# Optimization experiments

Measured on AMD Instinct MI355X. Metric: run time of the kernel, lower is better.

The kernel has to match this reference:

```python
import jax, jax.numpy as jnp
import numpy as np

B, S, F = 128, 1024, 512
H = 32          # LSTM hidden size
G = 4 * H       # i, f, g, o gates


def setup_inputs() -> dict:
    key = jax.random.key(0)
    ks = jax.random.split(key, 12)
    sc = lambda fan_in: 1.0 / np.sqrt(fan_in)
    return {
        "x":  jax.random.normal(ks[0], (B, S, F), dtype=jnp.float32),
        "W1": jax.random.normal(ks[1], (F, 32), dtype=jnp.float32) * sc(F),
        "b1": jnp.zeros((32,), jnp.float32),
        "W2": jax.random.normal(ks[2], (32, 64), dtype=jnp.float32) * sc(32),
        "b2": jnp.zeros((64,), jnp.float32),
        "Wx": jax.random.normal(ks[3], (64, G), dtype=jnp.float32) * sc(64),
        "Wh": jax.random.normal(ks[4], (H, G), dtype=jnp.float32) * sc(H),
        "bl": jnp.zeros((G,), jnp.float32),
        "W3": jax.random.normal(ks[5], (H, 64), dtype=jnp.float32) * sc(H),
        "b3": jnp.zeros((64,), jnp.float32),
        "W4": jax.random.normal(ks[6], (64, 512), dtype=jnp.float32) * sc(64),
        "b4": jnp.zeros((512,), jnp.float32),
    }


def _lstm_scan(xg, Wh):
    # xg: [B, S, 4H] precomputed input-side gate pre-activations (incl. bias)
    def step(carry, xt):
        c, h = carry
        g = xt + h @ Wh                      # [B, 4H]
        i, f, gg, o = jnp.split(g, 4, axis=-1)
        i, f, o = jax.nn.sigmoid(i), jax.nn.sigmoid(f), jax.nn.sigmoid(o)
        c = f * c + i * jnp.tanh(gg)
        h = o * jnp.tanh(c)
        return (c, h), h

    c0 = jnp.zeros((xg.shape[0], H), xg.dtype)
    h0 = jnp.zeros((xg.shape[0], H), xg.dtype)
    _, hs = jax.lax.scan(step, (c0, h0), jnp.swapaxes(xg, 0, 1))  # hs: [S, B, H]
    return jnp.swapaxes(hs, 0, 1)            # [B, S, H]


def reference(x, W1, b1, W2, b2, Wx, Wh, bl, W3, b3, W4, b4):
    h = jnp.tanh(x @ W1 + b1)                # [B, S, 32]
    h = jnp.tanh(h @ W2 + b2)                # [B, S, 64]
    xg = h @ Wx + bl                          # [B, S, 4H] input-side gates
    hs = _lstm_scan(xg, Wh)                   # [B, S, H]
    h = jnp.tanh(hs @ W3 + b3)                # [B, S, 64]
    return h @ W4 + b4                        # [B, S, 512]
```

## Files before the change

### kernel.cpp

```cpp
#include <hip/hip_runtime.h>
#include <hip/hip_bf16.h>


typedef __attribute__((ext_vector_type(8))) __bf16 bf16x8;
typedef __attribute__((ext_vector_type(4))) __bf16 bf16x4;
typedef __attribute__((ext_vector_type(4))) float floatx4;
typedef __attribute__((ext_vector_type(2))) float floatx2;

__global__ __launch_bounds__(256) void k_mlp_xg(
    const float* __restrict__ x,  const float* __restrict__ W1, const float* __restrict__ b1,
    const float* __restrict__ W2, const float* __restrict__ b2,
    const float* __restrict__ Wx, const float* __restrict__ bl,
    float* __restrict__ xg)
{
    __shared__ __align__(16) char smem[51712];
    __bf16* w1T = (__bf16*)smem;
    __bf16* w2T = (__bf16*)smem;
    __bf16* wxT = (__bf16*)(smem + 5120);
    __bf16* xsh = (__bf16*)(smem + 33280);
    __bf16* xsl = (__bf16*)(smem + 42496);
    __bf16* h1s = (__bf16*)(smem + 33280);
    __bf16* h2s = (__bf16*)(smem + 38400);

    const int tid  = threadIdx.x;
    const int lane = tid & 63, w = tid >> 6;
    const int quad = lane >> 4, col = lane & 15;
    const int row0 = blockIdx.x * 64;
    const int m     = w * 16 + col;
    const int rbase = w * 16 + quad * 4;
    const floatx4 fzero = {0.f, 0.f, 0.f, 0.f};

    for (int i = tid; i < 512 * 32; i += 256) {
        int k = i >> 5, n = i & 31;
        w1T[n * 520 + k] = (__bf16)W1[i];
    }
    auto stage_x = [&](int kc) {
        for (int i4 = tid; i4 < 1024; i4 += 256) {
            int f = i4 << 2; int r = f >> 6, cc = f & 63;
            float4 v = *(const float4*)(x + (size_t)(row0 + r) * 512 + kc * 64 + cc);
            __bf16 h0 = (__bf16)v.x, h1 = (__bf16)v.y, h2 = (__bf16)v.z, h3 = (__bf16)v.w;
            bf16x4 hi = {h0, h1, h2, h3};
            bf16x4 lo = {(__bf16)(v.x - (float)h0), (__bf16)(v.y - (float)h1),
                         (__bf16)(v.z - (float)h2), (__bf16)(v.w - (float)h3)};
            *(bf16x4*)(xsh + r * 72 + cc) = hi;
            *(bf16x4*)(xsl + r * 72 + cc) = lo;
        }
    };
    stage_x(0);
    __syncthreads();

    floatx4 acc1[2] = {fzero, fzero};
    for (int kc = 0; kc < 8; ++kc) {
#pragma unroll
        for (int ks = 0; ks < 2; ++ks) {
            int ko = ks * 32 + quad * 8;
            bf16x8 ah = *(const bf16x8*)(xsh + m * 72 + ko);
            bf16x8 al = *(const bf16x8*)(xsl + m * 72 + ko);
            int kg = kc * 64 + ko;
#pragma unroll
            for (int nt = 0; nt < 2; ++nt) {
                bf16x8 bfr = *(const bf16x8*)(w1T + (nt * 16 + col) * 520 + kg);
                acc1[nt] = __builtin_amdgcn_mfma_f32_16x16x32_bf16(ah, bfr, acc1[nt], 0, 0, 0);
                acc1[nt] = __builtin_amdgcn_mfma_f32_16x16x32_bf16(al, bfr, acc1[nt], 0, 0, 0);
            }
        }
        if (kc < 7) { __syncthreads(); stage_x(kc + 1); __syncthreads(); }
    }
    __syncthreads();

#pragma unroll
    for (int nt = 0; nt < 2; ++nt) {
        float bb = b1[nt * 16 + col];
#pragma unroll
        for (int r = 0; r < 4; ++r)
            h1s[(rbase + r) * 40 + nt * 16 + col] = (__bf16)tanhf(acc1[nt][r] + bb);
    }
    for (int i = tid; i < 32 * 64; i += 256)  { int k = i >> 6, n = i & 63;  w2T[n * 40 + k] = (__bf16)W2[i]; }
    for (int i = tid; i < 64 * 128; i += 256) { int k = i >> 7, n = i & 127; wxT[n * 72 + k] = (__bf16)Wx[i]; }
    __syncthreads();

    bf16x8 a2 = *(const bf16x8*)(h1s + m * 40 + quad * 8);
    floatx4 acc2[4];
#pragma unroll
    for (int nt = 0; nt < 4; ++nt) {
        bf16x8 bfr = *(const bf16x8*)(w2T + (nt * 16 + col) * 40 + quad * 8);
        acc2[nt] = __builtin_amdgcn_mfma_f32_16x16x32_bf16(a2, bfr, fzero, 0, 0, 0);
    }
#pragma unroll
    for (int nt = 0; nt < 4; ++nt) {
        float bb = b2[nt * 16 + col];
#pragma unroll
        for (int r = 0; r < 4; ++r)
            h2s[(rbase + r) * 72 + nt * 16 + col] = (__bf16)tanhf(acc2[nt][r] + bb);
    }

    floatx4 acc3[8];
#pragma unroll
    for (int nt = 0; nt < 8; ++nt) acc3[nt] = fzero;
#pragma unroll
    for (int ks = 0; ks < 2; ++ks) {
        int ko = ks * 32 + quad * 8;
        bf16x8 a3 = *(const bf16x8*)(h2s + m * 72 + ko);
#pragma unroll
        for (int nt = 0; nt < 8; ++nt) {
            bf16x8 bfr = *(const bf16x8*)(wxT + (nt * 16 + col) * 72 + ko);
            acc3[nt] = __builtin_amdgcn_mfma_f32_16x16x32_bf16(a3, bfr, acc3[nt], 0, 0, 0);
        }
    }
#pragma unroll
    for (int nt = 0; nt < 8; ++nt) {
        float bb = bl[nt * 16 + col];
#pragma unroll
        for (int r = 0; r < 4; ++r)
            xg[(size_t)(row0 + rbase + r) * 128 + nt * 16 + col] = acc3[nt][r] + bb;
    }
}

#define RLANE(v, k) __uint_as_float(__builtin_amdgcn_readlane(__float_as_uint(v), (k)))

__global__ __launch_bounds__(64) void k_lstm(
    const float* __restrict__ xg, const float* __restrict__ Wh,
    float* __restrict__ hs)
{
    __shared__ __align__(16) float xbuf[3][32 * 128];

    const int b = blockIdx.x;
    const int l = threadIdx.x;
    const float* xgb = xg + (size_t)b * 1024 * 128;
    float* hsb = hs + (size_t)b * 1024 * 32;

    floatx2 wh[32];
#pragma unroll
    for (int k = 0; k < 32; ++k)
        wh[k] = floatx2{Wh[k * 128 + l], Wh[k * 128 + 64 + l]};

    const float sc1 = (l < 32) ? 2.0f : 1.0f;
    const float m1  = (l < 32) ? 2.0f : 1.0f;
    const float c1  = (l < 32) ? -1.0f : 0.0f;

    auto stage_chunk = [&](int cidx) {
        const float* src = xgb + (size_t)cidx * 4096 + l * 4;
        float* dst = &xbuf[cidx % 3][0];
#pragma unroll
        for (int i = 0; i < 16; ++i)
            __builtin_amdgcn_global_load_lds(src + i * 256, dst + i * 256, 16, 0, 0);
    };

    stage_chunk(0); stage_chunk(1); stage_chunk(2);
    asm volatile("s_waitcnt vmcnt(16)" ::: "memory");

    float c = 0.f, h = 0.f;

    float xr0[4], xr1[4];
#pragma unroll
    for (int p = 0; p < 4; ++p) {
        xr0[p] = xbuf[0][p * 128 + l];
        xr1[p] = xbuf[0][p * 128 + 64 + l];
    }

#pragma unroll 1
    for (int ch = 0; ch < 32; ++ch) {
        const float* bufc = xbuf[ch % 3];
        const float* bufn = xbuf[(ch + 1) % 3];
#pragma unroll 1
        for (int s = 0; s < 32; s += 4) {
#pragma unroll
            for (int u = 0; u < 4; ++u) {
                const int tc = ch * 32 + s + u;
                float x0 = xr0[u], x1 = xr1[u];
                {
                    int rn = s + u + 4;
                    const float* p = (rn < 32) ? (bufc + rn * 128) : (bufn + (rn - 32) * 128);
                    xr0[u] = p[l];
                    xr1[u] = p[64 + l];
                }
                floatx2 pa = {x0, x1};
                floatx2 pb = {0.f, 0.f}, pc = {0.f, 0.f}, pd = {0.f, 0.f};
#pragma unroll
                for (int k = 0; k < 32; k += 4) {
                    float h0 = RLANE(h, k);
                    float h1 = RLANE(h, k + 1);
                    float h2 = RLANE(h, k + 2);
                    float h3 = RLANE(h, k + 3);
                    pa += wh[k]     * h0;
                    pb += wh[k + 1] * h1;
                    pc += wh[k + 2] * h2;
                    pd += wh[k + 3] * h3;
                }
                floatx2 pe = (pa + pb) + (pc + pd);
                float pre0 = pe.x;
                float pre1 = pe.y;
                float a0 = __builtin_amdgcn_rcpf(1.0f + __expf(-pre0));
                float s1 = __builtin_amdgcn_rcpf(1.0f + __expf(-sc1 * pre1));
                float a1 = __builtin_fmaf(s1, m1, c1);
                float f_ = __shfl(a0, l ^ 32);
                float o_ = __shfl(a1, l ^ 32);
                c = f_ * c + a0 * a1;
                float e = __expf(-2.0f * c);
                float th = (1.0f - e) * __builtin_amdgcn_rcpf(1.0f + e);
                h = o_ * th;
                if (l < 32) hsb[tc * 32 + l] = h;
            }
        }
        if (ch + 3 < 32) {
            stage_chunk(ch + 3);
            asm volatile("s_waitcnt vmcnt(16)" ::: "memory");
        } else {
            asm volatile("s_waitcnt vmcnt(0)" ::: "memory");
        }
    }
}

__global__ __launch_bounds__(256) void k_tail(
    const float* __restrict__ hs, const float* __restrict__ W3, const float* __restrict__ b3,
    const float* __restrict__ W4, const float* __restrict__ b4,
    float* __restrict__ out)
{
    __shared__ __align__(16) char smem[37888];
    __bf16* hss = (__bf16*)smem;
    __bf16* w3T = (__bf16*)(smem + 5120);
    __bf16* h3s = (__bf16*)(smem + 10240);
    __bf16* w4T = (__bf16*)(smem + 19456);

    const int tid  = threadIdx.x;
    const int lane = tid & 63, w = tid >> 6;
    const int quad = lane >> 4, col = lane & 15;
    const int row0 = blockIdx.x * 64;
    const int m     = w * 16 + col;
    const int rbase = w * 16 + quad * 4;
    const floatx4 fzero = {0.f, 0.f, 0.f, 0.f};

    for (int i4 = tid; i4 < 512; i4 += 256) {
        int f = i4 << 2; int r = f >> 5, cc = f & 31;
        float4 v = *(const float4*)(hs + (size_t)(row0 + r) * 32 + cc);
        bf16x4 hv = {(__bf16)v.x, (__bf16)v.y, (__bf16)v.z, (__bf16)v.w};
        *(bf16x4*)(hss + r * 40 + cc) = hv;
    }
    for (int i = tid; i < 32 * 64; i += 256) { int k = i >> 6, n = i & 63; w3T[n * 40 + k] = (__bf16)W3[i]; }
    __syncthreads();

    bf16x8 a3 = *(const bf16x8*)(hss + m * 40 + quad * 8);
    floatx4 acc3[4];
#pragma unroll
    for (int nt = 0; nt < 4; ++nt) {
        bf16x8 bfr = *(const bf16x8*)(w3T + (nt * 16 + col) * 40 + quad * 8);
        acc3[nt] = __builtin_amdgcn_mfma_f32_16x16x32_bf16(a3, bfr, fzero, 0, 0, 0);
    }
#pragma unroll
    for (int nt = 0; nt < 4; ++nt) {
        float bb = b3[nt * 16 + col];
#pragma unroll
        for (int r = 0; r < 4; ++r)
            h3s[(rbase + r) * 72 + nt * 16 + col] = (__bf16)tanhf(acc3[nt][r] + bb);
    }

    for (int oc = 0; oc < 4; ++oc) {
        __syncthreads();
        for (int i4 = tid; i4 < 2048; i4 += 256) {
            int f = i4 << 2; int k = f >> 7, cc = f & 127;
            float4 v = *(const float4*)(W4 + (size_t)k * 512 + oc * 128 + cc);
            w4T[(cc + 0) * 72 + k] = (__bf16)v.x;
            w4T[(cc + 1) * 72 + k] = (__bf16)v.y;
            w4T[(cc + 2) * 72 + k] = (__bf16)v.z;
            w4T[(cc + 3) * 72 + k] = (__bf16)v.w;
        }
        __syncthreads();

        floatx4 acc4[8];
#pragma unroll
        for (int nt = 0; nt < 8; ++nt) acc4[nt] = fzero;
#pragma unroll
        for (int ks = 0; ks < 2; ++ks) {
            int ko = ks * 32 + quad * 8;
            bf16x8 a4 = *(const bf16x8*)(h3s + m * 72 + ko);
#pragma unroll
            for (int nt = 0; nt < 8; ++nt) {
                bf16x8 bfr = *(const bf16x8*)(w4T + (nt * 16 + col) * 72 + ko);
                acc4[nt] = __builtin_amdgcn_mfma_f32_16x16x32_bf16(a4, bfr, acc4[nt], 0, 0, 0);
            }
        }
#pragma unroll
        for (int nt = 0; nt < 8; ++nt) {
            float bb = b4[oc * 128 + nt * 16 + col];
#pragma unroll
            for (int r = 0; r < 4; ++r)
                out[(size_t)(row0 + rbase + r) * 512 + oc * 128 + nt * 16 + col] = acc4[nt][r] + bb;
        }
    }
}

extern "C" void kernel_launch(void* const* d_in, const int* in_sizes, int n_in,
                              void* d_out, int out_size, void* d_ws, size_t ws_size,
                              hipStream_t stream)
{
    (void)in_sizes; (void)n_in; (void)out_size;
    const float* x  = (const float*)d_in[0];
    const float* W1 = (const float*)d_in[1];
    const float* b1 = (const float*)d_in[2];
    const float* W2 = (const float*)d_in[3];
    const float* b2 = (const float*)d_in[4];
    const float* Wx = (const float*)d_in[5];
    const float* Wh = (const float*)d_in[6];
    const float* bl = (const float*)d_in[7];
    const float* W3 = (const float*)d_in[8];
    const float* b3 = (const float*)d_in[9];
    const float* W4 = (const float*)d_in[10];
    const float* b4 = (const float*)d_in[11];
    float* out = (float*)d_out;

    const size_t hsElems = (size_t)128 * 1024 * 32;
    const size_t xgElems = (size_t)128 * 1024 * 128;
    float* hs = (float*)d_ws;
    float* xg = (ws_size >= (hsElems + xgElems) * sizeof(float))
                    ? hs + hsElems
                    : out;

    k_mlp_xg<<<2048, 256, 0, stream>>>(x, W1, b1, W2, b2, Wx, bl, xg);
    k_lstm<<<128, 64, 0, stream>>>(xg, Wh, hs);
    k_tail<<<2048, 256, 0, stream>>>(hs, W3, b3, W4, b4, out);
}
```

Baseline: 830.9 us.

## Load x directly into MFMA fragments and enlarge tail kernel row tiles

Result: no change. 818.9 us (-1.4%).

```diff
diff --git a/kernel.cpp b/kernel.cpp
--- a/kernel.cpp
+++ b/kernel.cpp
@@ -13,12 +13,10 @@
     const float* __restrict__ Wx, const float* __restrict__ bl,
     float* __restrict__ xg)
 {
-    __shared__ __align__(16) char smem[51712];
+    __shared__ __align__(16) char smem[47616];
     __bf16* w1T = (__bf16*)smem;
     __bf16* w2T = (__bf16*)smem;
     __bf16* wxT = (__bf16*)(smem + 5120);
-    __bf16* xsh = (__bf16*)(smem + 33280);
-    __bf16* xsl = (__bf16*)(smem + 42496);
     __bf16* h1s = (__bf16*)(smem + 33280);
     __bf16* h2s = (__bf16*)(smem + 38400);
 
@@ -34,29 +32,23 @@
         int k = i >> 5, n = i & 31;
         w1T[n * 520 + k] = (__bf16)W1[i];
     }
-    auto stage_x = [&](int kc) {
-        for (int i4 = tid; i4 < 1024; i4 += 256) {
-            int f = i4 << 2; int r = f >> 6, cc = f & 63;
-            float4 v = *(const float4*)(x + (size_t)(row0 + r) * 512 + kc * 64 + cc);
-            __bf16 h0 = (__bf16)v.x, h1 = (__bf16)v.y, h2 = (__bf16)v.z, h3 = (__bf16)v.w;
-            bf16x4 hi = {h0, h1, h2, h3};
-            bf16x4 lo = {(__bf16)(v.x - (float)h0), (__bf16)(v.y - (float)h1),
-                         (__bf16)(v.z - (float)h2), (__bf16)(v.w - (float)h3)};
-            *(bf16x4*)(xsh + r * 72 + cc) = hi;
-            *(bf16x4*)(xsl + r * 72 + cc) = lo;
-        }
-    };
-    stage_x(0);
     __syncthreads();
 
+    const float* xrow = x + (size_t)(row0 + m) * 512;
     floatx4 acc1[2] = {fzero, fzero};
     for (int kc = 0; kc < 8; ++kc) {
 #pragma unroll
         for (int ks = 0; ks < 2; ++ks) {
-            int ko = ks * 32 + quad * 8;
-            bf16x8 ah = *(const bf16x8*)(xsh + m * 72 + ko);
-            bf16x8 al = *(const bf16x8*)(xsl + m * 72 + ko);
-            int kg = kc * 64 + ko;
+            int kg = kc * 64 + ks * 32 + quad * 8;
+            float4 v0 = *(const float4*)(xrow + kg);
+            float4 v1 = *(const float4*)(xrow + kg + 4);
+            __bf16 e0 = (__bf16)v0.x, e1 = (__bf16)v0.y, e2 = (__bf16)v0.z, e3 = (__bf16)v0.w;
+            __bf16 e4 = (__bf16)v1.x, e5 = (__bf16)v1.y, e6 = (__bf16)v1.z, e7 = (__bf16)v1.w;
+            bf16x8 ah = {e0, e1, e2, e3, e4, e5, e6, e7};
+            bf16x8 al = {(__bf16)(v0.x - (float)e0), (__bf16)(v0.y - (float)e1),
+                         (__bf16)(v0.z - (float)e2), (__bf16)(v0.w - (float)e3),
+                         (__bf16)(v1.x - (float)e4), (__bf16)(v1.y - (float)e5),
+                         (__bf16)(v1.z - (float)e6), (__bf16)(v1.w - (float)e7)};
 #pragma unroll
             for (int nt = 0; nt < 2; ++nt) {
                 bf16x8 bfr = *(const bf16x8*)(w1T + (nt * 16 + col) * 520 + kg);
@@ -64,7 +56,6 @@
                 acc1[nt] = __builtin_amdgcn_mfma_f32_16x16x32_bf16(al, bfr, acc1[nt], 0, 0, 0);
             }
         }
-        if (kc < 7) { __syncthreads(); stage_x(kc + 1); __syncthreads(); }
     }
     __syncthreads();
 
@@ -211,26 +202,24 @@
     }
 }
 
-__global__ __launch_bounds__(256) void k_tail(
+__global__ __launch_bounds__(256, 2) void k_tail(
     const float* __restrict__ hs, const float* __restrict__ W3, const float* __restrict__ b3,
     const float* __restrict__ W4, const float* __restrict__ b4,
     float* __restrict__ out)
 {
-    __shared__ __align__(16) char smem[37888];
-    __bf16* hss = (__bf16*)smem;
-    __bf16* w3T = (__bf16*)(smem + 5120);
-    __bf16* h3s = (__bf16*)(smem + 10240);
-    __bf16* w4T = (__bf16*)(smem + 19456);
+    __shared__ __align__(16) char smem[62464];
+    __bf16* h3s = (__bf16*)smem;
+    __bf16* hss = (__bf16*)(smem + 36864);
+    __bf16* w4T = (__bf16*)(smem + 36864);
+    __bf16* w3T = (__bf16*)(smem + 57344);
 
     const int tid  = threadIdx.x;
     const int lane = tid & 63, w = tid >> 6;
     const int quad = lane >> 4, col = lane & 15;
-    const int row0 = blockIdx.x * 64;
-    const int m     = w * 16 + col;
-    const int rbase = w * 16 + quad * 4;
+    const int row0 = blockIdx.x * 256;
     const floatx4 fzero = {0.f, 0.f, 0.f, 0.f};
 
-    for (int i4 = tid; i4 < 512; i4 += 256) {
+    for (int i4 = tid; i4 < 2048; i4 += 256) {
         int f = i4 << 2; int r = f >> 5, cc = f & 31;
         float4 v = *(const float4*)(hs + (size_t)(row0 + r) * 32 + cc);
         bf16x4 hv = {(__bf16)v.x, (__bf16)v.y, (__bf16)v.z, (__bf16)v.w};
@@ -239,52 +228,75 @@
     for (int i = tid; i < 32 * 64; i += 256) { int k = i >> 6, n = i & 63; w3T[n * 40 + k] = (__bf16)W3[i]; }
     __syncthreads();
 
-    bf16x8 a3 = *(const bf16x8*)(hss + m * 40 + quad * 8);
-    floatx4 acc3[4];
-#pragma unroll
-    for (int nt = 0; nt < 4; ++nt) {
-        bf16x8 bfr = *(const bf16x8*)(w3T + (nt * 16 + col) * 40 + quad * 8);
-        acc3[nt] = __builtin_amdgcn_mfma_f32_16x16x32_bf16(a3, bfr, fzero, 0, 0, 0);
-    }
-#pragma unroll
-    for (int nt = 0; nt < 4; ++nt) {
-        float bb = b3[nt * 16 + col];
-#pragma unroll
-        for (int r = 0; r < 4; ++r)
-            h3s[(rbase + r) * 72 + nt * 16 + col] = (__bf16)tanhf(acc3[nt][r] + bb);
+#pragma unroll
+    for (int mt = 0; mt < 4; ++mt) {
+        const int m     = w * 64 + mt * 16 + col;
+        const int rbase = w * 64 + mt * 16 + quad * 4;
+        bf16x8 a3 = *(const bf16x8*)(hss + m * 40 + quad * 8);
+        floatx4 acc3[4];
+#pragma unroll
+        for (int nt = 0; nt < 4; ++nt) {
+            bf16x8 bfr = *(const bf16x8*)(w3T + (nt * 16 + col) * 40 + quad * 8);
+            acc3[nt] = __builtin_amdgcn_mfma_f32_16x16x32_bf16(a3, bfr, fzero, 0, 0, 0);
+        }
+#pragma unroll
+        for (int nt = 0; nt < 4; ++nt) {
+            float bb = b3[nt * 16 + col];
+#pragma unroll
+            for (int r = 0; r < 4; ++r)
+                h3s[(rbase + r) * 72 + nt * 16 + col] = (__bf16)tanhf(acc3[nt][r] + bb);
+        }
     }
 
     for (int oc = 0; oc < 4; ++oc) {
         __syncthreads();
-        for (int i4 = tid; i4 < 2048; i4 += 256) {
-            int f = i4 << 2; int k = f >> 7, cc = f & 127;
-            float4 v = *(const float4*)(W4 + (size_t)k * 512 + oc * 128 + cc);
-            w4T[(cc + 0) * 72 + k] = (__bf16)v.x;
-            w4T[(cc + 1) * 72 + k] = (__bf16)v.y;
-            w4T[(cc + 2) * 72 + k] = (__bf16)v.z;
-            w4T[(cc + 3) * 72 + k] = (__bf16)v.w;
+        for (int it = tid; it < 512; it += 256) {
+            int k0 = (it >> 5) << 2;
+            int n0 = (it & 31) << 2;
+            const float* wp = W4 + (size_t)k0 * 512 + oc * 128 + n0;
+            float4 r0 = *(const float4*)(wp);
+            float4 r1 = *(const float4*)(wp + 512);
+            float4 r2 = *(const float4*)(wp + 1024);
+            float4 r3 = *(const float4*)(wp + 1536);
+            bf16x4 c0 = {(__bf16)r0.x, (__bf16)r1.x, (__bf16)r2.x, (__bf16)r3.x};
+            bf16x4 c1 = {(__bf16)r0.y, (__bf16)r1.y, (__bf16)r2.y, (__bf16)r3.y};
+            bf16x4 c2 = {(__bf16)r0.z, (__bf16)r1.z, (__bf16)r2.z, (__bf16)r3.z};
+            bf16x4 c3 = {(__bf16)r0.w, (__bf16)r1.w, (__bf16)r2.w, (__bf16)r3.w};
+            *(bf16x4*)(w4T + (n0 + 0) * 76 + k0) = c0;
+            *(bf16x4*)(w4T + (n0 + 1) * 76 + k0) = c1;
+            *(bf16x4*)(w4T + (n0 + 2) * 76 + k0) = c2;
+            *(bf16x4*)(w4T + (n0 + 3) * 76 + k0) = c3;
         }
         __syncthreads();
 
-        floatx4 acc4[8];
-#pragma unroll
-        for (int nt = 0; nt < 8; ++nt) acc4[nt] = fzero;
+        floatx4 acc4[4][8];
+#pragma unroll
+        for (int mt = 0; mt < 4; ++mt)
+#pragma unroll
+            for (int nt = 0; nt < 8; ++nt) acc4[mt][nt] = fzero;
 #pragma unroll
         for (int ks = 0; ks < 2; ++ks) {
             int ko = ks * 32 + quad * 8;
-            bf16x8 a4 = *(const bf16x8*)(h3s + m * 72 + ko);
-#pragma unroll
-            for (int nt = 0; nt < 8; ++nt) {
-                bf16x8 bfr = *(const bf16x8*)(w4T + (nt * 16 + col) * 72 + ko);
-                acc4[nt] = __builtin_amdgcn_mfma_f32_16x16x32_bf16(a4, bfr, acc4[nt], 0, 0, 0);
+#pragma unroll
+            for (int mt = 0; mt < 4; ++mt) {
+                bf16x8 a4 = *(const bf16x8*)(h3s + (w * 64 + mt * 16 + col) * 72 + ko);
+#pragma unroll
+                for (int nt = 0; nt < 8; ++nt) {
+                    bf16x8 bfr = *(const bf16x8*)(w4T + (nt * 16 + col) * 76 + ko);
+                    acc4[mt][nt] = __builtin_amdgcn_mfma_f32_16x16x32_bf16(a4, bfr, acc4[mt][nt], 0, 0, 0);
+                }
             }
         }
 #pragma unroll
         for (int nt = 0; nt < 8; ++nt) {
             float bb = b4[oc * 128 + nt * 16 + col];
 #pragma unroll
-            for (int r = 0; r < 4; ++r)
-                out[(size_t)(row0 + rbase + r) * 512 + oc * 128 + nt * 16 + col] = acc4[nt][r] + bb;
+            for (int mt = 0; mt < 4; ++mt) {
+                const int rbase = row0 + w * 64 + mt * 16 + quad * 4;
+#pragma unroll
+                for (int r = 0; r < 4; ++r)
+                    out[(size_t)(rbase + r) * 512 + oc * 128 + nt * 16 + col] = acc4[mt][nt][r] + bb;
+            }
         }
     }
 }
@@ -317,5 +329,5 @@
 
     k_mlp_xg<<<2048, 256, 0, stream>>>(x, W1, b1, W2, b2, Wx, bl, xg);
     k_lstm<<<128, 64, 0, stream>>>(xg, Wh, hs);
-    k_tail<<<2048, 256, 0, stream>>>(hs, W3, b3, W4, b4, out);
+    k_tail<<<512, 256, 0, stream>>>(hs, W3, b3, W4, b4, out);
 }
```
